# Kernel tuning notes

Measured on AMD Instinct MI355X. Metric: run time of the kernel, lower is better.

## Reference

```python
import jax, jax.numpy as jnp
import numpy as np
from jax import lax

B, T, C, H, W = 2, 32, 8, 192, 192


def _conv(x, w, b):
    y = lax.conv_general_dilated(x, w, (1, 1), 'SAME',
                                 dimension_numbers=('NCHW', 'OIHW', 'NCHW'))
    return y + b[None, :, None, None]


def _interaction(x, c1w, c1b, c2w, c2b, c3w, c3b):
    x = jax.nn.silu(_conv(x, c1w, c1b))
    x = jax.nn.silu(_conv(x, c2w, c2b))
    return _conv(x, c3w, c3b)


def _constrain(xf, ky, kx, k2):
    # xf: [B,T,C,H,Wf] complex; divergence-free projection on channels 0 (u) and 1 (v)
    u = xf[:, :, 0]
    v = xf[:, :, 1]
    div = (ky[:, None] * u + kx[None, :] * v) / k2
    xf = xf.at[:, :, 0].set(u - ky[:, None] * div)
    xf = xf.at[:, :, 1].set(v - kx[None, :] * div)
    return xf


def setup_inputs() -> dict:
    key = jax.random.key(0)
    ks = jax.random.split(key, 8)
    f32 = jnp.float32
    return {
        'x_seq': jax.random.normal(ks[0], (B, T, C, H, W), f32),
        'dt': jax.random.uniform(ks[1], (B,), f32) * 0.1 + 0.01,
        'w1': jax.random.normal(ks[2], (2, 64), f32) * 0.02,
        'b1': jnp.zeros((64,), f32),
        'w2': jax.random.normal(ks[3], (64, C), f32) * 0.02,
        'b2': jnp.zeros((C,), f32),
        'c1w': jax.random.normal(ks[4], (2 * C, C, 3, 3), f32) * 0.05,
        'c1b': jnp.zeros((2 * C,), f32),
        'c2w': jax.random.normal(ks[5], (2 * C, 2 * C, 3, 3), f32) * 0.05,
        'c2b': jnp.zeros((2 * C,), f32),
        'c3w': jax.random.normal(ks[6], (C, 2 * C, 1, 1), f32) * 0.05,
        'c3b': jnp.zeros((C,), f32),
    }


def reference(x_seq, dt, w1, b1, w2, b2, c1w, c1b, c2w, c2b, c3w, c3b):
    Bb, Tt, Cc, Hh, Ww = x_seq.shape
    Wf = Ww // 2 + 1
    ky = jnp.fft.fftfreq(Hh).astype(jnp.float32)
    kx = jnp.fft.rfftfreq(Ww).astype(jnp.float32)
    k2 = ky[:, None] ** 2 + kx[None, :] ** 2
    k2 = k2.at[0, 0].set(1.0)

    # --- learned propagator: A = exp(i * (MLP(k) + |k|) * dt) ---
    kg = jnp.stack(jnp.meshgrid(ky, kx, indexing='ij'), axis=-1).reshape(-1, 2)
    hid = jax.nn.silu(kg @ w1 + b1)
    learned_phase = (hid @ w2 + b2).reshape(Hh, Wf, Cc)
    k_phys = jnp.sqrt(ky[:, None] ** 2 + kx[None, :] ** 2)[..., None]  # [H,Wf,1]
    omega = learned_phase + k_phys
    phase = omega[None] * dt[:, None, None, None]  # [B,H,Wf,C]
    A = lax.complex(jnp.cos(phase), jnp.sin(phase))

    # --- analytical force: grad of interaction-net output sum wrt input ---
    x_flat = x_seq.reshape(Bb * Tt, Cc, Hh, Ww)
    force = jax.grad(lambda xx: _interaction(xx, c1w, c1b, c2w, c2b, c3w, c3b).sum())(x_flat)
    force = force.reshape(Bb, Tt, Cc, Hh, Ww)

    Xf = jnp.fft.rfft2(x_seq + force * dt[:, None, None, None, None],
                       axes=(-2, -1), norm='ortho')  # [B,T,C,H,Wf] complex
    Xf = _constrain(Xf, ky, kx, k2)

    # --- linear recurrence h_t = A*h_{t-1} + X_t via associative scan over T ---
    A_b = jnp.broadcast_to(jnp.transpose(A, (0, 3, 1, 2))[:, None], Xf.shape)

    def comb(e1, e2):
        a1, x1 = e1
        a2, x2 = e2
        return a1 * a2, a2 * x1 + x2

    _, h_f = lax.associative_scan(comb, (A_b, Xf), axis=1)
    h_f = _constrain(h_f, ky, kx, k2)

    # --- energy renormalization ---
    n_in = jnp.sqrt(jnp.sum(jnp.abs(Xf) ** 2, axis=(2, 3, 4), keepdims=True))
    n_out = jnp.sqrt(jnp.sum(jnp.abs(h_f) ** 2, axis=(2, 3, 4), keepdims=True))
    h_f = h_f * (n_in / (n_out + 1e-6))

    return jnp.fft.irfft2(h_f, s=(Hh, Ww), axes=(-2, -1), norm='ortho')
```

## Files before the change

### kernel.cpp

```cpp
#include <hip/hip_runtime.h>
#include <hip/hip_bf16.h>
#include <math.h>

#define HH 192
#define WW 192
#define WF 97
#define NC 8
#define NC2 16
#define NT 32
#define NB 2
#define NIMG (NB*NT)
#define NPLANE (NIMG*NC)
#define PIX (HH*WW)
#define FPIX (HH*WF)
#define NG 13
#define INV_SQRT_N 0.07216878364870322f
#define SCAN_BLOCKS (NB*NC*FPIX/256)

typedef __attribute__((ext_vector_type(8))) short bf16x8;
typedef __attribute__((ext_vector_type(4))) float f32x4;

__device__ inline unsigned short f2bf(float f){
    union { __hip_bfloat16 h; unsigned short u; } cv;
    cv.h = __float2bfloat16(f);
    return cv.u;
}
__device__ inline float bf2f(unsigned short h){
    return __uint_as_float(((unsigned int)h) << 16);
}
__device__ inline float fsigmoid(float y){
    return __builtin_amdgcn_rcpf(1.f + __expf(-y));
}

__global__ void k_tab(float* tw){
    int i = blockIdx.x*blockDim.x + threadIdx.x;
    if (i < 192){
        double ang = 6.283185307179586476925286766559 * (double)i / 192.0;
        tw[i]       = (float)cos(ang);
        tw[192 + i] = (float)sin(ang);
    }
}

__global__ void k_wprep(const float* __restrict__ c1w, const float* __restrict__ c2w,
                        const float* __restrict__ c3w,
                        unsigned short* __restrict__ WT, float* __restrict__ S3){
    int e = blockIdx.x*256 + threadIdx.x;
    if (e < 9216){
        int j  = e & 7;
        int l  = (e >> 3) & 63;
        int fs = e >> 9;
        int px = l & 15, ks = l >> 4;
        float w = 0.f;
        if (fs < 3){
            int tap = 4*fs + ks;
            if (tap < 9) w = c1w[(px*8 + j)*9 + tap];
        } else if (fs < 8){
            int s = fs - 3, tap = 2*s + (ks>>1);
            int ch = (ks&1)*8 + j;
            if (tap < 9) w = c2w[(px*16 + ch)*9 + tap];
        } else if (fs < 13){
            int s = fs - 8, tb = 2*s + (ks>>1);
            int c2 = (ks&1)*8 + j;
            if (tb < 9) w = c2w[(c2*16 + px)*9 + (8 - tb)];
        } else {
            int s = fs - 13, tb = 2*s + (ks>>1);
            int cin = (ks&1)*8 + j;
            if (tb < 9 && px < 8) w = c1w[(cin*8 + px)*9 + (8 - tb)];
        }
        WT[e] = f2bf(w);
    } else if (e < 9232){
        int och = e - 9216;
        float s3 = 0.f;
        for (int q = 0; q < NC; q++) s3 += c3w[q*NC2 + och];
        S3[och] = s3;
    }
}

__global__ void k_A(const float* __restrict__ dt, const float* __restrict__ w1,
                    const float* __restrict__ b1, const float* __restrict__ w2,
                    const float* __restrict__ b2, float* __restrict__ Abuf){
    int idx = blockIdx.x*blockDim.x + threadIdx.x;
    if (idx >= FPIX) return;
    int kyi = idx % HH, kxi = idx / HH;
    float ky = (float)(kyi < 96 ? kyi : kyi - 192) / 192.0f;
    float kx = (float)kxi / 192.0f;
    float lp[NC];
    #pragma unroll
    for (int c = 0; c < NC; c++) lp[c] = b2[c];
    for (int jh = 0; jh < 64; jh++){
        float z  = ky*w1[jh] + kx*w1[64+jh] + b1[jh];
        float sg = 1.0f/(1.0f + expf(-z));
        float h  = z*sg;
        #pragma unroll
        for (int c = 0; c < NC; c++) lp[c] += h * w2[jh*NC + c];
    }
    float kph = sqrtf(ky*ky + kx*kx);
    for (int b = 0; b < NB; b++){
        float d = dt[b];
        #pragma unroll
        for (int c = 0; c < NC; c++){
            float ph = (lp[c] + kph) * d;
            float s, cn;
            sincosf(ph, &s, &cn);
            long o = (((long)(b*NC + c))*FPIX + idx) * 2;
            Abuf[o]   = cn;
            Abuf[o+1] = s;
        }
    }
}

__global__ void k_force(const float* __restrict__ x,
                        const unsigned short* __restrict__ WTu,
                        const float* __restrict__ c1b, const float* __restrict__ c2b,
                        const float* __restrict__ S3,  const float* __restrict__ dt,
                        float* __restrict__ xp){
    __shared__ unsigned short ys1_s[22*22*16];
    __shared__ unsigned short xg2_s[20*20*16];
    int bid = blockIdx.x;
    int tx0 = (bid % 12)*16, ty0 = ((bid/12) % 12)*16;
    int img = bid / 144;
    int tid = threadIdx.x;
    int l = tid & 63, px = l & 15, ks = l >> 4, wv = tid >> 6;
    const bf16x8* wt = (const bf16x8*)WTu;

    unsigned short* xs = xg2_s;
    const float* xb = x + (long)img*NC*PIX;
    for (int pix = tid; pix < 576; pix += 256){
        int sy = pix / 24, sx = pix % 24;
        int gy = ty0 - 4 + sy, gx = tx0 - 4 + sx;
        bool vld = (gy >= 0 && gy < HH && gx >= 0 && gx < WW);
        long gp = (long)gy*WW + gx;
        ushort4 o0, o1;
        #pragma unroll
        for (int c = 0; c < 8; c++){
            float v = vld ? xb[c*PIX + gp] : 0.f;
            unsigned short h = f2bf(v);
            if (c < 4) ((unsigned short*)&o0)[c] = h;
            else       ((unsigned short*)&o1)[c-4] = h;
        }
        *(ushort4*)(xs + pix*8)     = o0;
        *(ushort4*)(xs + pix*8 + 4) = o1;
    }
    __syncthreads();

    ushort4 dy1r[6];
    {
        bf16x8 a0 = wt[0*64 + l], a1 = wt[1*64 + l], a2 = wt[2*64 + l];
        float b1v[4];
        #pragma unroll
        for (int r = 0; r < 4; r++) b1v[r] = c1b[ks*4 + r];
        int t0 = (0 + ks < 9) ? ks : 8;
        int t1 = (4 + ks < 9) ? 4 + ks : 8;
        int t2 = 8;
        int o0 = ((t0/3)*24 + t0%3)*8, o1 = ((t1/3)*24 + t1%3)*8, o2 = ((t2/3)*24 + t2%3)*8;
        #pragma unroll
        for (int i = 0; i < 6; i++){
            int g = wv + 4*i;
            if (g < 21){
                int p = g*16 + px;
                int pc = (p < 324) ? p : 323;
                int ry = pc/18, rx = pc%18;
                const unsigned short* bp = xs + ((ry+2)*24 + rx+2)*8;
                f32x4 acc = {0.f,0.f,0.f,0.f};
                acc = __builtin_amdgcn_mfma_f32_16x16x32_bf16(a0, *(const bf16x8*)(bp+o0), acc, 0,0,0);
                acc = __builtin_amdgcn_mfma_f32_16x16x32_bf16(a1, *(const bf16x8*)(bp+o1), acc, 0,0,0);
                acc = __builtin_amdgcn_mfma_f32_16x16x32_bf16(a2, *(const bf16x8*)(bp+o2), acc, 0,0,0);
                int gy = ty0 - 1 + ry, gx = tx0 - 1 + rx;
                bool vld = (gy >= 0 && gy < HH && gx >= 0 && gx < WW);
                ushort4 yo, dyo;
                #pragma unroll
                for (int r = 0; r < 4; r++){
                    float yv = acc[r] + b1v[r];
                    float sg = fsigmoid(yv);
                    ((unsigned short*)&yo)[r]  = vld ? f2bf(yv*sg) : (unsigned short)0;
                    ((unsigned short*)&dyo)[r] = vld ? f2bf(sg*(1.f + yv*(1.f - sg)))
                                                     : (unsigned short)0;
                }
                dy1r[i] = dyo;
                if (p < 324)
                    *(ushort4*)(ys1_s + ((ry+2)*22 + rx+2)*16 + ks*4) = yo;
            }
        }
        #pragma unroll
        for (int i = 0; i < 3; i++){
            int g = wv + 4*i;
            if (g < 10){
                int p = g*16 + px;
                int oy, ox;
                if (p < 88){ int q = p/22; oy = (q < 2) ? q : q + 18; ox = p - q*22; }
                else { int rr = p - 88; oy = (rr>>2) + 2; int c4 = rr & 3;
                       ox = (c4 < 2) ? c4 : c4 + 18; }
                const unsigned short* bp = xs + (oy*24 + ox)*8;
                f32x4 acc = {0.f,0.f,0.f,0.f};
                acc = __builtin_amdgcn_mfma_f32_16x16x32_bf16(a0, *(const bf16x8*)(bp+o0), acc, 0,0,0);
                acc = __builtin_amdgcn_mfma_f32_16x16x32_bf16(a1, *(const bf16x8*)(bp+o1), acc, 0,0,0);
                acc = __builtin_amdgcn_mfma_f32_16x16x32_bf16(a2, *(const bf16x8*)(bp+o2), acc, 0,0,0);
                int gy = ty0 - 3 + oy, gx = tx0 - 3 + ox;
                bool vld = (gy >= 0 && gy < HH && gx >= 0 && gx < WW);
                ushort4 yo;
                #pragma unroll
                for (int r = 0; r < 4; r++){
                    float yv = acc[r] + b1v[r];
                    float sg = fsigmoid(yv);
                    ((unsigned short*)&yo)[r] = vld ? f2bf(yv*sg) : (unsigned short)0;
                }
                *(ushort4*)(ys1_s + (oy*22 + ox)*16 + ks*4) = yo;
            }
        }
    }
    __syncthreads();

    unsigned short* g2s = xg2_s;
    {
        bf16x8 a0 = wt[3*64+l], a1 = wt[4*64+l], a2 = wt[5*64+l],
               a3 = wt[6*64+l], a4 = wt[7*64+l];
        float b2v[4], s3v[4];
        #pragma unroll
        for (int r = 0; r < 4; r++){ b2v[r] = c2b[ks*4+r]; s3v[r] = S3[ks*4+r]; }
        int hb = (ks&1)*8;
        int toff[5];
        #pragma unroll
        for (int s = 0; s < 5; s++){
            int tap = 2*s + (ks>>1); int t = (tap < 9) ? tap : 8;
            toff[s] = ((t/3)*22 + t%3)*16 + hb;
        }
        #pragma unroll
        for (int i = 0; i < 7; i++){
            int g = wv + 4*i;
            if (g < 25){
                int p = g*16 + px;
                int qy = p/20, qx = p%20;
                const unsigned short* bp = ys1_s + (qy*22 + qx)*16;
                f32x4 acc = {0.f,0.f,0.f,0.f};
                acc = __builtin_amdgcn_mfma_f32_16x16x32_bf16(a0, *(const bf16x8*)(bp+toff[0]), acc, 0,0,0);
                acc = __builtin_amdgcn_mfma_f32_16x16x32_bf16(a1, *(const bf16x8*)(bp+toff[1]), acc, 0,0,0);
                acc = __builtin_amdgcn_mfma_f32_16x16x32_bf16(a2, *(const bf16x8*)(bp+toff[2]), acc, 0,0,0);
                acc = __builtin_amdgcn_mfma_f32_16x16x32_bf16(a3, *(const bf16x8*)(bp+toff[3]), acc, 0,0,0);
                acc = __builtin_amdgcn_mfma_f32_16x16x32_bf16(a4, *(const bf16x8*)(bp+toff[4]), acc, 0,0,0);
                int gy = ty0 - 2 + qy, gx = tx0 - 2 + qx;
                bool vld = (gy >= 0 && gy < HH && gx >= 0 && gx < WW);
                ushort4 go;
                #pragma unroll
                for (int r = 0; r < 4; r++){
                    float yv = acc[r] + b2v[r];
                    float sg = fsigmoid(yv);
                    float ds = sg*(1.f + yv*(1.f - sg));
                    ((unsigned short*)&go)[r] = vld ? f2bf(ds * s3v[r]) : (unsigned short)0;
                }
                *(ushort4*)(g2s + p*16 + ks*4) = go;
            }
        }
    }
    __syncthreads();

    unsigned short* g1s = ys1_s;
    {
        bf16x8 a0 = wt[8*64+l], a1 = wt[9*64+l], a2 = wt[10*64+l],
               a3 = wt[11*64+l], a4 = wt[12*64+l];
        int hb = (ks&1)*8;
        int toff[5];
        #pragma unroll
        for (int s = 0; s < 5; s++){
            int tb = 2*s + (ks>>1); int t = (tb < 9) ? tb : 8;
            toff[s] = ((2-(t/3))*20 + 2-(t%3))*16 + hb;
        }
        #pragma unroll
        for (int i = 0; i < 6; i++){
            int g = wv + 4*i;
            if (g < 21){
                int p = g*16 + px;
                int pc = (p < 324) ? p : 323;
                int ry = pc/18, rx = pc%18;
                const unsigned short* bp = g2s + (ry*20 + rx)*16;
                f32x4 acc = {0.f,0.f,0.f,0.f};
                acc = __builtin_amdgcn_mfma_f32_16x16x32_bf16(a0, *(const bf16x8*)(bp+toff[0]), acc, 0,0,0);
                acc = __builtin_amdgcn_mfma_f32_16x16x32_bf16(a1, *(const bf16x8*)(bp+toff[1]), acc, 0,0,0);
                acc = __builtin_amdgcn_mfma_f32_16x16x32_bf16(a2, *(const bf16x8*)(bp+toff[2]), acc, 0,0,0);
                acc = __builtin_amdgcn_mfma_f32_16x16x32_bf16(a3, *(const bf16x8*)(bp+toff[3]), acc, 0,0,0);
                acc = __builtin_amdgcn_mfma_f32_16x16x32_bf16(a4, *(const bf16x8*)(bp+toff[4]), acc, 0,0,0);
                if (p < 324){
                    ushort4 dv = dy1r[i];
                    ushort4 go;
                    #pragma unroll
                    for (int r = 0; r < 4; r++){
                        float v = acc[r] * bf2f(((unsigned short*)&dv)[r]);
                        ((unsigned short*)&go)[r] = f2bf(v);
                    }
                    *(ushort4*)(g1s + p*16 + ks*4) = go;
                }
            }
        }
    }
    __syncthreads();

    {
        bf16x8 a0 = wt[13*64+l], a1 = wt[14*64+l], a2 = wt[15*64+l],
               a3 = wt[16*64+l], a4 = wt[17*64+l];
        int hb = (ks&1)*8;
        int toff[5];
        #pragma unroll
        for (int s = 0; s < 5; s++){
            int tb = 2*s + (ks>>1); int t = (tb < 9) ? tb : 8;
            toff[s] = ((2-(t/3))*18 + 2-(t%3))*16 + hb;
        }
        float d = dt[img / NT];
        #pragma unroll
        for (int i = 0; i < 4; i++){
            int y = wv + 4*i;
            const unsigned short* bp = g1s + (y*18 + px)*16;
            f32x4 acc = {0.f,0.f,0.f,0.f};
            acc = __builtin_amdgcn_mfma_f32_16x16x32_bf16(a0, *(const bf16x8*)(bp+toff[0]), acc, 0,0,0);
            acc = __builtin_amdgcn_mfma_f32_16x16x32_bf16(a1, *(const bf16x8*)(bp+toff[1]), acc, 0,0,0);
            acc = __builtin_amdgcn_mfma_f32_16x16x32_bf16(a2, *(const bf16x8*)(bp+toff[2]), acc, 0,0,0);
            acc = __builtin_amdgcn_mfma_f32_16x16x32_bf16(a3, *(const bf16x8*)(bp+toff[3]), acc, 0,0,0);
            acc = __builtin_amdgcn_mfma_f32_16x16x32_bf16(a4, *(const bf16x8*)(bp+toff[4]), acc, 0,0,0);
            if (ks < 2){
                int gpix = (ty0+y)*WW + (tx0+px);
                #pragma unroll
                for (int r = 0; r < 4; r++){
                    int c = ks*4 + r;
                    long gi = ((long)img*NC + c)*PIX + gpix;
                    xp[gi] = x[gi] + d*acc[r];
                }
            }
        }
    }
}

__global__ void k_rowfft2(const float* __restrict__ xp, const float* __restrict__ tw,
                          float* __restrict__ R){
    __shared__ float2 bufC[1728];
    __shared__ float2 bufA[1836];
    __shared__ float twc[192], tws[192];
    int p  = blockIdx.x / 12;
    int r0 = (blockIdx.x % 12)*16;
    int t  = threadIdx.x;
    twc[t] = tw[t]; tws[t] = tw[192+t];
    const float* base = xp + (long)p*PIX + (long)r0*WW;
    #pragma unroll
    for (int jj = 0; jj < 8; jj++){
        float2 z; z.x = base[(2*jj)*WW + t]; z.y = base[(2*jj+1)*WW + t];
        bufC[t*9 + jj] = z;
    }
    __syncthreads();
    int k1 = t / 12, n2 = t % 12;
    {
        float wr[16], wi[16];
        int m = (n2*k1) % 192, step = (12*k1) % 192;
        #pragma unroll
        for (int n1 = 0; n1 < 16; n1++){
            wr[n1] = twc[m]; wi[n1] = -tws[m];
            m += step; if (m >= 192) m -= 192;
        }
        #pragma unroll
        for (int jj = 0; jj < 8; jj++){
            float re = 0.f, im = 0.f;
            #pragma unroll
            for (int n1 = 0; n1 < 16; n1++){
                float2 v = bufC[(12*n1 + n2)*9 + jj];
                re += v.x*wr[n1] - v.y*wi[n1];
                im += v.x*wi[n1] + v.y*wr[n1];
            }
            float2 a; a.x = re; a.y = im;
            bufA[(n2*17 + k1)*9 + jj] = a;
        }
    }
    __syncthreads();
    {
        int kk1 = t % 16, k2 = t / 16;
        float wr[12], wi[12];
        int m = 0, step = (16*k2) % 192;
        #pragma unroll
        for (int q = 0; q < 12; q++){
            wr[q] = twc[m]; wi[q] = -tws[m];
            m += step; if (m >= 192) m -= 192;
        }
        #pragma unroll
        for (int jj = 0; jj < 8; jj++){
            float re = 0.f, im = 0.f;
            #pragma unroll
            for (int q = 0; q < 12; q++){
                float2 a = bufA[(q*17 + kk1)*9 + jj];
                re += a.x*wr[q] - a.y*wi[q];
                im += a.x*wi[q] + a.y*wr[q];
            }
            float2 z; z.x = re*INV_SQRT_N; z.y = im*INV_SQRT_N;
            bufC[t*9 + jj] = z;
        }
    }
    __syncthreads();
    if (t < WF){
        int t2 = (t == 0) ? 0 : 192 - t;
        #pragma unroll
        for (int jj = 0; jj < 8; jj++){
            float2 u = bufC[t*9 + jj], v = bufC[t2*9 + jj];
            float2 A_; A_.x = 0.5f*(u.x + v.x); A_.y = 0.5f*(u.y - v.y);
            float2 B_; B_.x = 0.5f*(u.y + v.y); B_.y = -0.5f*(u.x - v.x);
            bufA[t*17 + 2*jj]     = A_;
            bufA[t*17 + 2*jj + 1] = B_;
        }
    }
    __syncthreads();
    float2* dst = ((float2*)R) + (long)p*FPIX + r0;
    for (int idx = t; idx < 97*16; idx += 192){
        int kx = idx >> 4, ry = idx & 15;
        dst[(long)kx*HH + ry] = bufA[kx*17 + ry];
    }
}

__global__ void k_invrow2(const float* __restrict__ G, const float* __restrict__ tw,
                          float* __restrict__ out){
    __shared__ float2 bufC[1728];
    __shared__ float2 bufA[1836];
    __shared__ float twc[192], tws[192];
    int p  = blockIdx.x / 12;
    int r0 = (blockIdx.x % 12)*16;
    int t  = threadIdx.x;
    twc[t] = tw[t]; tws[t] = tw[192+t];
    const float2* Gb = ((const float2*)G) + (long)p*FPIX + r0;
    for (int idx = t; idx < 97*16; idx += 192){
        int kx = idx >> 4, ry = idx & 15;
        bufA[kx*17 + ry] = Gb[(long)kx*HH + ry];
    }
    __syncthreads();
    int tt = (t <= 96) ? t : 192 - t;
    bool dcny = (t == 0) || (t == 96);
    #pragma unroll
    for (int jj = 0; jj < 8; jj++){
        float2 a = bufA[tt*17 + 2*jj];
        float2 b = bufA[tt*17 + 2*jj + 1];
        if (dcny){ a.y = 0.f; b.y = 0.f; }
        float2 z;
        if (t <= 96){ z.x = a.x - b.y; z.y = a.y + b.x; }
        else        { z.x = a.x + b.y; z.y = b.x - a.y; }
        bufC[t*9 + jj] = z;
    }
    __syncthreads();
    int k1 = t / 12, n2 = t % 12;
    {
        float wr[16], wi[16];
        int m = (n2*k1) % 192, step = (12*k1) % 192;
        #pragma unroll
        for (int n1 = 0; n1 < 16; n1++){
            wr[n1] = twc[m]; wi[n1] = tws[m];
            m += step; if (m >= 192) m -= 192;
        }
        #pragma unroll
        for (int jj = 0; jj < 8; jj++){
            float re = 0.f, im = 0.f;
            #pragma unroll
            for (int n1 = 0; n1 < 16; n1++){
                float2 v = bufC[(12*n1 + n2)*9 + jj];
                re += v.x*wr[n1] - v.y*wi[n1];
                im += v.x*wi[n1] + v.y*wr[n1];
            }
            float2 a; a.x = re; a.y = im;
            bufA[(n2*17 + k1)*9 + jj] = a;
        }
    }
    __syncthreads();
    {
        int kk1 = t % 16, k2 = t / 16;
        float wr[12], wi[12];
        int m = 0, step = (16*k2) % 192;
        #pragma unroll
        for (int q = 0; q < 12; q++){
            wr[q] = twc[m]; wi[q] = tws[m];
            m += step; if (m >= 192) m -= 192;
        }
        float* ob = out + (long)p*PIX + (long)r0*WW;
        #pragma unroll
        for (int jj = 0; jj < 8; jj++){
            float re = 0.f, im = 0.f;
            #pragma unroll
            for (int q = 0; q < 12; q++){
                float2 a = bufA[(q*17 + kk1)*9 + jj];
                re += a.x*wr[q] - a.y*wi[q];
                im += a.x*wi[q] + a.y*wr[q];
            }
            ob[(2*jj)*WW + t]   = re*INV_SQRT_N;
            ob[(2*jj+1)*WW + t] = im*INV_SQRT_N;
        }
    }
}

template<int DIRSGN, bool RESCALE>
__global__ void k_cfft(const float* __restrict__ in, const float* __restrict__ tw,
                       const float* __restrict__ nrm, float* __restrict__ out){
    __shared__ float2 C[HH][9];
    __shared__ float2 A1[12][17][9];
    __shared__ float twc[192], tws[192];
    const float sgn = (DIRSGN > 0) ? 1.f : -1.f;
    int p  = blockIdx.x / NG;
    int g  = blockIdx.x % NG;
    int j0 = g*8;
    int t  = threadIdx.x;
    twc[t] = tw[t]; tws[t] = tw[192+t];
    float scale = 1.f;
    if (RESCALE){
        int bt = p / NC;
        scale = sqrtf(nrm[bt]) / (sqrtf(nrm[64+bt]) + 1e-6f);
    }
    const float2* src = ((const float2*)in) + (long)p*FPIX;
    #pragma unroll
    for (int jj = 0; jj < 8; jj++){
        float2 v = {0.f, 0.f};
        if (j0 + jj < WF) v = src[(long)(j0+jj)*HH + t];
        v.x *= scale; v.y *= scale;
        C[t][jj] = v;
    }
    __syncthreads();
    {
        int k1 = t / 12, n2 = t % 12;
        float wr[16], wi[16];
        int m = (n2*k1) % 192, step = (12*k1) % 192;
        #pragma unroll
        for (int n1 = 0; n1 < 16; n1++){
            wr[n1] = twc[m]; wi[n1] = sgn*tws[m];
            m += step; if (m >= 192) m -= 192;
        }
        #pragma unroll
        for (int jj = 0; jj < 8; jj++){
            float re = 0.f, im = 0.f;
            #pragma unroll
            for (int n1 = 0; n1 < 16; n1++){
                float2 v = C[12*n1 + n2][jj];
                re += v.x*wr[n1] - v.y*wi[n1];
                im += v.x*wi[n1] + v.y*wr[n1];
            }
            float2 a; a.x = re; a.y = im;
            A1[n2][k1][jj] = a;
        }
    }
    __syncthreads();
    {
        int k1 = t % 16, k2 = t / 16;
        float wr[12], wi[12];
        int m = 0, step = (16*k2) % 192;
        #pragma unroll
        for (int n2 = 0; n2 < 12; n2++){
            wr[n2] = twc[m]; wi[n2] = sgn*tws[m];
            m += step; if (m >= 192) m -= 192;
        }
        float2* dst = ((float2*)out) + (long)p*FPIX;
        #pragma unroll
        for (int jj = 0; jj < 8; jj++){
            float re = 0.f, im = 0.f;
            #pragma unroll
            for (int n2 = 0; n2 < 12; n2++){
                float2 a = A1[n2][k1][jj];
                re += a.x*wr[n2] - a.y*wi[n2];
                im += a.x*wi[n2] + a.y*wr[n2];
            }
            if (j0 + jj < WF){
                float2 r; r.x = re*INV_SQRT_N; r.y = im*INV_SQRT_N;
                dst[(long)(j0+jj)*HH + t] = r;
            }
        }
    }
}

__global__ void k_scan(const float* __restrict__ Xf, const float* __restrict__ Abuf,
                       float* __restrict__ Hf, float* __restrict__ scr){
    __shared__ float part[64];
    int tid = threadIdx.x;
    if (tid < 64) part[tid] = 0.f;
    __syncthreads();
    int idx = blockIdx.x*256 + tid;
    int f = idx % FPIX; int tmp = idx / FPIX;
    int c = tmp % NC; int b = tmp / NC;
    int lane0 = ((tid & 63) == 0);
    if (c == 0){
        int kyi = f % HH, kxi = f / HH;
        float ky = (float)(kyi < 96 ? kyi : kyi - 192)/192.0f;
        float kx = (float)kxi/192.0f;
        float k2 = ky*ky + kx*kx;
        if (f == 0) k2 = 1.0f;
        float rk2 = 1.0f/k2;
        long a0 = (((long)(b*NC + 0))*FPIX + f)*2;
        long a1 = (((long)(b*NC + 1))*FPIX + f)*2;
        float A0r = Abuf[a0], A0i = Abuf[a0+1];
        float A1r = Abuf[a1], A1i = Abuf[a1+1];
        float h0r = 0.f, h0i = 0.f, h1r = 0.f, h1i = 0.f;
        for (int t = 0; t < NT; t++){
            long e0 = (((((long)b*NT + t)*NC + 0)*FPIX) + f)*2;
            long e1 = (((((long)b*NT + t)*NC + 1)*FPIX) + f)*2;
            float ur = Xf[e0], ui = Xf[e0+1];
            float vr = Xf[e1], vi = Xf[e1+1];
            float pr = (ky*ur + kx*vr)*rk2;
            float pi = (ky*ui + kx*vi)*rk2;
            ur -= ky*pr; ui -= ky*pi;
            vr -= kx*pr; vi -= kx*pi;
            float nin = ur*ur + ui*ui + vr*vr + vi*vi;
            float n0r = A0r*h0r - A0i*h0i + ur;
            float n0i = A0r*h0i + A0i*h0r + ui;
            float n1r = A1r*h1r - A1i*h1i + vr;
            float n1i = A1r*h1i + A1i*h1r + vi;
            h0r = n0r; h0i = n0i; h1r = n1r; h1i = n1i;
            float dr = (ky*h0r + kx*h1r)*rk2;
            float di = (ky*h0i + kx*h1i)*rk2;
            float o0r = h0r - ky*dr, o0i = h0i - ky*di;
            float o1r = h1r - kx*dr, o1i = h1i - kx*di;
            Hf[e0] = o0r; Hf[e0+1] = o0i;
            Hf[e1] = o1r; Hf[e1+1] = o1i;
            float nout = o0r*o0r + o0i*o0i + o1r*o1r + o1i*o1i;
            #pragma unroll
            for (int off = 32; off > 0; off >>= 1){
                nin  += __shfl_xor(nin,  off);
                nout += __shfl_xor(nout, off);
            }
            if (lane0){
                atomicAdd(&part[t],      nin);
                atomicAdd(&part[32 + t], nout);
            }
        }
    } else if (c != 1){
        long ao = (((long)(b*NC + c))*FPIX + f)*2;
        float ar = Abuf[ao], ai = Abuf[ao+1];
        float hr = 0.0f, hi = 0.0f;
        for (int t = 0; t < NT; t++){
            long e = (((((long)b*NT + t)*NC + c)*FPIX) + f)*2;
            float xr = Xf[e], xi = Xf[e+1];
            float nin = xr*xr + xi*xi;
            float nr = ar*hr - ai*hi + xr;
            float ni = ar*hi + ai*hr + xi;
            hr = nr; hi = ni;
            Hf[e] = hr; Hf[e+1] = hi;
            float nout = hr*hr + hi*hi;
            #pragma unroll
            for (int off = 32; off > 0; off >>= 1){
                nin  += __shfl_xor(nin,  off);
                nout += __shfl_xor(nout, off);
            }
            if (lane0){
                atomicAdd(&part[t],      nin);
                atomicAdd(&part[32 + t], nout);
            }
        }
    }
    __syncthreads();
    if (tid < 64) scr[(long)blockIdx.x*64 + tid] = part[tid];
}

__global__ void k_nred(const float* __restrict__ scr, float* __restrict__ nrm){
    int o = threadIdx.x;
    int io = o >> 6;
    int bt = o & 63;
    int b = bt >> 5, t = bt & 31;
    const int BPB = SCAN_BLOCKS/NB;
    float s = 0.f;
    for (int blk = 0; blk < BPB; blk++)
        s += scr[((long)(b*BPB + blk))*64 + io*32 + t];
    nrm[io*64 + bt] = s;
}

extern "C" void kernel_launch(void* const* d_in, const int* in_sizes, int n_in,
                              void* d_out, int out_size, void* d_ws, size_t ws_size,
                              hipStream_t stream){
    const float* x   = (const float*)d_in[0];
    const float* dt  = (const float*)d_in[1];
    const float* w1  = (const float*)d_in[2];
    const float* b1  = (const float*)d_in[3];
    const float* w2  = (const float*)d_in[4];
    const float* b2  = (const float*)d_in[5];
    const float* c1w = (const float*)d_in[6];
    const float* c1b = (const float*)d_in[7];
    const float* c2w = (const float*)d_in[8];
    const float* c2b = (const float*)d_in[9];
    const float* c3w = (const float*)d_in[10];
    float* out = (float*)d_out;
    float* ws  = (float*)d_ws;

    const long RSZ = (long)NPLANE*FPIX*2;
    float* R1  = ws;
    float* R2  = ws + RSZ;
    float* AB  = R2 + RSZ;
    float* TW  = AB + (long)NB*NC*FPIX*2;
    float* NRM = TW + 384;
    float* WTf = NRM + 128;
    unsigned short* WT = (unsigned short*)WTf;
    float* S3  = WTf + 4608;
    float* SCR = S3 + 16;

    k_tab<<<2, 128, 0, stream>>>(TW);
    k_wprep<<<37, 256, 0, stream>>>(c1w, c2w, c3w, WT, S3);
    k_A<<<(FPIX + 255)/256, 256, 0, stream>>>(dt, w1, b1, w2, b2, AB);

    k_force<<<NIMG*144, 256, 0, stream>>>(x, WT, c1b, c2b, S3, dt, out);

    k_rowfft2<<<NPLANE*12, 192, 0, stream>>>(out, TW, R1);
    k_cfft<-1,false><<<NPLANE*NG, 192, 0, stream>>>(R1, TW, NRM, R2);
    k_scan<<<SCAN_BLOCKS, 256, 0, stream>>>(R2, AB, R1, SCR);
    k_nred<<<1, 128, 0, stream>>>(SCR, NRM);
    k_cfft<+1,true><<<NPLANE*NG, 192, 0, stream>>>(R1, TW, NRM, R2);
    k_invrow2<<<NPLANE*12, 192, 0, stream>>>(R2, TW, out);
}
```

Measured before the change: 604.9 us.

## Precompute per-thread twiddle tables and process two frequencies per scan thread

Adds a kernel that precomputes, for each forward/inverse direction, the per-thread twiddle factors used by the row and column FFT kernels. The FFT kernels now load them as coalesced float2 reads from global memory instead of staging cos/sin tables in shared memory and walking modular indices. The scan kernel now handles two adjacent frequencies per thread with float4 loads and stores, halving the thread count and widening memory accesses. This costs extra global twiddle traffic and more registers per scan thread, which lowers the number of scan blocks.

```diff
diff --git a/kernel.cpp b/kernel.cpp
--- a/kernel.cpp
+++ b/kernel.cpp
@@ -13,9 +13,10 @@
 #define NPLANE (NIMG*NC)
 #define PIX (HH*WW)
 #define FPIX (HH*WF)
+#define HP (FPIX/2)
 #define NG 13
 #define INV_SQRT_N 0.07216878364870322f
-#define SCAN_BLOCKS (NB*NC*FPIX/256)
+#define SCAN_BLOCKS (NB*NC*HP/256)
 
 typedef __attribute__((ext_vector_type(8))) short bf16x8;
 typedef __attribute__((ext_vector_type(4))) float f32x4;
@@ -39,6 +40,18 @@
         tw[i]       = (float)cos(ang);
         tw[192 + i] = (float)sin(ang);
     }
+}
+
+__global__ void k_twt(const float* __restrict__ tw, float2* __restrict__ twt){
+    int e = blockIdx.x*256 + threadIdx.x;
+    if (e >= 10752) return;
+    int t = e % 192; int s = (e/192) % 28; int d = e / (192*28);
+    float sgn = d ? 1.f : -1.f;
+    int m;
+    if (s < 16){ int k1 = t/12, n2 = t%12; m = (n2*k1 + 12*k1*s) % 192; }
+    else       { int q = s - 16; int k2 = t/16; m = (16*k2*q) % 192; }
+    float2 w; w.x = tw[m]; w.y = sgn*tw[192 + m];
+    twt[(d*28 + s)*192 + t] = w;
 }
 
 __global__ void k_wprep(const float* __restrict__ c1w, const float* __restrict__ c2w,
@@ -327,15 +340,13 @@
     }
 }
 
-__global__ void k_rowfft2(const float* __restrict__ xp, const float* __restrict__ tw,
+__global__ void k_rowfft2(const float* __restrict__ xp, const float2* __restrict__ twt,
                           float* __restrict__ R){
     __shared__ float2 bufC[1728];
     __shared__ float2 bufA[1836];
-    __shared__ float twc[192], tws[192];
     int p  = blockIdx.x / 12;
     int r0 = (blockIdx.x % 12)*16;
     int t  = threadIdx.x;
-    twc[t] = tw[t]; tws[t] = tw[192+t];
     const float* base = xp + (long)p*PIX + (long)r0*WW;
     #pragma unroll
     for (int jj = 0; jj < 8; jj++){
@@ -346,11 +357,10 @@
     int k1 = t / 12, n2 = t % 12;
     {
         float wr[16], wi[16];
-        int m = (n2*k1) % 192, step = (12*k1) % 192;
         #pragma unroll
         for (int n1 = 0; n1 < 16; n1++){
-            wr[n1] = twc[m]; wi[n1] = -tws[m];
-            m += step; if (m >= 192) m -= 192;
+            float2 w = twt[n1*192 + t];
+            wr[n1] = w.x; wi[n1] = w.y;
         }
         #pragma unroll
         for (int jj = 0; jj < 8; jj++){
@@ -367,13 +377,12 @@
     }
     __syncthreads();
     {
-        int kk1 = t % 16, k2 = t / 16;
+        int kk1 = t % 16;
         float wr[12], wi[12];
-        int m = 0, step = (16*k2) % 192;
         #pragma unroll
         for (int q = 0; q < 12; q++){
-            wr[q] = twc[m]; wi[q] = -tws[m];
-            m += step; if (m >= 192) m -= 192;
+            float2 w = twt[(16+q)*192 + t];
+            wr[q] = w.x; wi[q] = w.y;
         }
         #pragma unroll
         for (int jj = 0; jj < 8; jj++){
@@ -408,15 +417,13 @@
     }
 }
 
-__global__ void k_invrow2(const float* __restrict__ G, const float* __restrict__ tw,
+__global__ void k_invrow2(const float* __restrict__ G, const float2* __restrict__ twt,
                           float* __restrict__ out){
     __shared__ float2 bufC[1728];
     __shared__ float2 bufA[1836];
-    __shared__ float twc[192], tws[192];
     int p  = blockIdx.x / 12;
     int r0 = (blockIdx.x % 12)*16;
     int t  = threadIdx.x;
-    twc[t] = tw[t]; tws[t] = tw[192+t];
     const float2* Gb = ((const float2*)G) + (long)p*FPIX + r0;
     for (int idx = t; idx < 97*16; idx += 192){
         int kx = idx >> 4, ry = idx & 15;
@@ -437,13 +444,13 @@
     }
     __syncthreads();
     int k1 = t / 12, n2 = t % 12;
+    const float2* T = twt + 28*192;
     {
         float wr[16], wi[16];
-        int m = (n2*k1) % 192, step = (12*k1) % 192;
         #pragma unroll
         for (int n1 = 0; n1 < 16; n1++){
-            wr[n1] = twc[m]; wi[n1] = tws[m];
-            m += step; if (m >= 192) m -= 192;
+            float2 w = T[n1*192 + t];
+            wr[n1] = w.x; wi[n1] = w.y;
         }
         #pragma unroll
         for (int jj = 0; jj < 8; jj++){
@@ -460,13 +467,12 @@
     }
     __syncthreads();
     {
-        int kk1 = t % 16, k2 = t / 16;
+        int kk1 = t % 16;
         float wr[12], wi[12];
-        int m = 0, step = (16*k2) % 192;
         #pragma unroll
         for (int q = 0; q < 12; q++){
-            wr[q] = twc[m]; wi[q] = tws[m];
-            m += step; if (m >= 192) m -= 192;
+            float2 w = T[(16+q)*192 + t];
+            wr[q] = w.x; wi[q] = w.y;
         }
         float* ob = out + (long)p*PIX + (long)r0*WW;
         #pragma unroll
@@ -485,17 +491,15 @@
 }
 
 template<int DIRSGN, bool RESCALE>
-__global__ void k_cfft(const float* __restrict__ in, const float* __restrict__ tw,
+__global__ void k_cfft(const float* __restrict__ in, const float2* __restrict__ twt,
                        const float* __restrict__ nrm, float* __restrict__ out){
     __shared__ float2 C[HH][9];
     __shared__ float2 A1[12][17][9];
-    __shared__ float twc[192], tws[192];
-    const float sgn = (DIRSGN > 0) ? 1.f : -1.f;
+    const int DIRI = (DIRSGN > 0) ? 1 : 0;
     int p  = blockIdx.x / NG;
     int g  = blockIdx.x % NG;
     int j0 = g*8;
     int t  = threadIdx.x;
-    twc[t] = tw[t]; tws[t] = tw[192+t];
     float scale = 1.f;
     if (RESCALE){
         int bt = p / NC;
@@ -510,14 +514,14 @@
         C[t][jj] = v;
     }
     __syncthreads();
+    const float2* T = twt + DIRI*28*192;
     {
         int k1 = t / 12, n2 = t % 12;
         float wr[16], wi[16];
-        int m = (n2*k1) % 192, step = (12*k1) % 192;
         #pragma unroll
         for (int n1 = 0; n1 < 16; n1++){
-            wr[n1] = twc[m]; wi[n1] = sgn*tws[m];
-            m += step; if (m >= 192) m -= 192;
+            float2 w = T[n1*192 + t];
+            wr[n1] = w.x; wi[n1] = w.y;
         }
         #pragma unroll
         for (int jj = 0; jj < 8; jj++){
@@ -534,23 +538,22 @@
     }
     __syncthreads();
     {
-        int k1 = t % 16, k2 = t / 16;
+        int k1 = t % 16;
         float wr[12], wi[12];
-        int m = 0, step = (16*k2) % 192;
-        #pragma unroll
-        for (int n2 = 0; n2 < 12; n2++){
-            wr[n2] = twc[m]; wi[n2] = sgn*tws[m];
-            m += step; if (m >= 192) m -= 192;
+        #pragma unroll
+        for (int q = 0; q < 12; q++){
+            float2 w = T[(16+q)*192 + t];
+            wr[q] = w.x; wi[q] = w.y;
         }
         float2* dst = ((float2*)out) + (long)p*FPIX;
         #pragma unroll
         for (int jj = 0; jj < 8; jj++){
             float re = 0.f, im = 0.f;
             #pragma unroll
-            for (int n2 = 0; n2 < 12; n2++){
-                float2 a = A1[n2][k1][jj];
-                re += a.x*wr[n2] - a.y*wi[n2];
-                im += a.x*wi[n2] + a.y*wr[n2];
+            for (int q = 0; q < 12; q++){
+                float2 a = A1[q][k1][jj];
+                re += a.x*wr[q] - a.y*wi[q];
+                im += a.x*wi[q] + a.y*wr[q];
             }
             if (j0 + jj < WF){
                 float2 r; r.x = re*INV_SQRT_N; r.y = im*INV_SQRT_N;
@@ -567,43 +570,64 @@
     if (tid < 64) part[tid] = 0.f;
     __syncthreads();
     int idx = blockIdx.x*256 + tid;
-    int f = idx % FPIX; int tmp = idx / FPIX;
+    int u = idx % HP; int tmp = idx / HP;
     int c = tmp % NC; int b = tmp / NC;
+    int f0 = 2*u;
     int lane0 = ((tid & 63) == 0);
     if (c == 0){
-        int kyi = f % HH, kxi = f / HH;
-        float ky = (float)(kyi < 96 ? kyi : kyi - 192)/192.0f;
-        float kx = (float)kxi/192.0f;
-        float k2 = ky*ky + kx*kx;
-        if (f == 0) k2 = 1.0f;
-        float rk2 = 1.0f/k2;
-        long a0 = (((long)(b*NC + 0))*FPIX + f)*2;
-        long a1 = (((long)(b*NC + 1))*FPIX + f)*2;
-        float A0r = Abuf[a0], A0i = Abuf[a0+1];
-        float A1r = Abuf[a1], A1i = Abuf[a1+1];
-        float h0r = 0.f, h0i = 0.f, h1r = 0.f, h1i = 0.f;
+        int ky0i = f0 % HH, kxi = f0 / HH;
+        float ky0 = (float)(ky0i < 96 ? ky0i : ky0i - 192)/192.0f;
+        int ky1i = ky0i + 1;
+        float ky1 = (float)(ky1i < 96 ? ky1i : ky1i - 192)/192.0f;
+        float kx_ = (float)kxi/192.0f;
+        float k20 = ky0*ky0 + kx_*kx_; if (f0 == 0) k20 = 1.0f;
+        float k21 = ky1*ky1 + kx_*kx_;
+        float rk20 = 1.0f/k20, rk21 = 1.0f/k21;
+        long a0 = (((long)(b*NC + 0))*FPIX + f0)*2;
+        long a1 = (((long)(b*NC + 1))*FPIX + f0)*2;
+        float4 A0 = *(const float4*)(Abuf + a0);
+        float4 A1v = *(const float4*)(Abuf + a1);
+        float h0r0=0.f,h0i0=0.f,h1r0=0.f,h1i0=0.f;
+        float h0r1=0.f,h0i1=0.f,h1r1=0.f,h1i1=0.f;
         for (int t = 0; t < NT; t++){
-            long e0 = (((((long)b*NT + t)*NC + 0)*FPIX) + f)*2;
-            long e1 = (((((long)b*NT + t)*NC + 1)*FPIX) + f)*2;
-            float ur = Xf[e0], ui = Xf[e0+1];
-            float vr = Xf[e1], vi = Xf[e1+1];
-            float pr = (ky*ur + kx*vr)*rk2;
-            float pi = (ky*ui + kx*vi)*rk2;
-            ur -= ky*pr; ui -= ky*pi;
-            vr -= kx*pr; vi -= kx*pi;
+            long e0 = (((((long)b*NT + t)*NC + 0)*FPIX) + f0)*2;
+            long e1 = (((((long)b*NT + t)*NC + 1)*FPIX) + f0)*2;
+            float4 U = *(const float4*)(Xf + e0);
+            float4 V = *(const float4*)(Xf + e1);
+            float ur = U.x, ui = U.y, vr = V.x, vi = V.y;
+            float pr = (ky0*ur + kx_*vr)*rk20;
+            float pi = (ky0*ui + kx_*vi)*rk20;
+            ur -= ky0*pr; ui -= ky0*pi; vr -= kx_*pr; vi -= kx_*pi;
             float nin = ur*ur + ui*ui + vr*vr + vi*vi;
-            float n0r = A0r*h0r - A0i*h0i + ur;
-            float n0i = A0r*h0i + A0i*h0r + ui;
-            float n1r = A1r*h1r - A1i*h1i + vr;
-            float n1i = A1r*h1i + A1i*h1r + vi;
-            h0r = n0r; h0i = n0i; h1r = n1r; h1i = n1i;
-            float dr = (ky*h0r + kx*h1r)*rk2;
-            float di = (ky*h0i + kx*h1i)*rk2;
-            float o0r = h0r - ky*dr, o0i = h0i - ky*di;
-            float o1r = h1r - kx*dr, o1i = h1i - kx*di;
-            Hf[e0] = o0r; Hf[e0+1] = o0i;
-            Hf[e1] = o1r; Hf[e1+1] = o1i;
+            float n0r = A0.x*h0r0 - A0.y*h0i0 + ur;
+            float n0i = A0.x*h0i0 + A0.y*h0r0 + ui;
+            float n1r = A1v.x*h1r0 - A1v.y*h1i0 + vr;
+            float n1i = A1v.x*h1i0 + A1v.y*h1r0 + vi;
+            h0r0 = n0r; h0i0 = n0i; h1r0 = n1r; h1i0 = n1i;
+            float dr = (ky0*h0r0 + kx_*h1r0)*rk20;
+            float di = (ky0*h0i0 + kx_*h1i0)*rk20;
+            float o0r = h0r0 - ky0*dr, o0i = h0i0 - ky0*di;
+            float o1r = h1r0 - kx_*dr, o1i = h1i0 - kx_*di;
             float nout = o0r*o0r + o0i*o0i + o1r*o1r + o1i*o1i;
+            float ur1 = U.z, ui1 = U.w, vr1 = V.z, vi1 = V.w;
+            float pr1 = (ky1*ur1 + kx_*vr1)*rk21;
+            float pi1 = (ky1*ui1 + kx_*vi1)*rk21;
+            ur1 -= ky1*pr1; ui1 -= ky1*pi1; vr1 -= kx_*pr1; vi1 -= kx_*pi1;
+            nin += ur1*ur1 + ui1*ui1 + vr1*vr1 + vi1*vi1;
+            float m0r = A0.z*h0r1 - A0.w*h0i1 + ur1;
+            float m0i = A0.z*h0i1 + A0.w*h0r1 + ui1;
+            float m1r = A1v.z*h1r1 - A1v.w*h1i1 + vr1;
+            float m1i = A1v.z*h1i1 + A1v.w*h1r1 + vi1;
+            h0r1 = m0r; h0i1 = m0i; h1r1 = m1r; h1i1 = m1i;
+            float dr1 = (ky1*h0r1 + kx_*h1r1)*rk21;
+            float di1 = (ky1*h0i1 + kx_*h1i1)*rk21;
+            float q0r = h0r1 - ky1*dr1, q0i = h0i1 - ky1*di1;
+            float q1r = h1r1 - kx_*dr1, q1i = h1i1 - kx_*di1;
+            nout += q0r*q0r + q0i*q0i + q1r*q1r + q1i*q1i;
+            float4 O0; O0.x = o0r; O0.y = o0i; O0.z = q0r; O0.w = q0i;
+            float4 O1; O1.x = o1r; O1.y = o1i; O1.z = q1r; O1.w = q1i;
+            *(float4*)(Hf + e0) = O0;
+            *(float4*)(Hf + e1) = O1;
             #pragma unroll
             for (int off = 32; off > 0; off >>= 1){
                 nin  += __shfl_xor(nin,  off);
@@ -615,18 +639,21 @@
             }
         }
     } else if (c != 1){
-        long ao = (((long)(b*NC + c))*FPIX + f)*2;
-        float ar = Abuf[ao], ai = Abuf[ao+1];
-        float hr = 0.0f, hi = 0.0f;
+        long ao = (((long)(b*NC + c))*FPIX + f0)*2;
+        float4 A = *(const float4*)(Abuf + ao);
+        float hr0 = 0.f, hi0 = 0.f, hr1 = 0.f, hi1 = 0.f;
         for (int t = 0; t < NT; t++){
-            long e = (((((long)b*NT + t)*NC + c)*FPIX) + f)*2;
-            float xr = Xf[e], xi = Xf[e+1];
-            float nin = xr*xr + xi*xi;
-            float nr = ar*hr - ai*hi + xr;
-            float ni = ar*hi + ai*hr + xi;
-            hr = nr; hi = ni;
-            Hf[e] = hr; Hf[e+1] = hi;
-            float nout = hr*hr + hi*hi;
+            long e = (((((long)b*NT + t)*NC + c)*FPIX) + f0)*2;
+            float4 X = *(const float4*)(Xf + e);
+            float nin = X.x*X.x + X.y*X.y + X.z*X.z + X.w*X.w;
+            float nr0 = A.x*hr0 - A.y*hi0 + X.x;
+            float ni0 = A.x*hi0 + A.y*hr0 + X.y;
+            float nr1 = A.z*hr1 - A.w*hi1 + X.z;
+            float ni1 = A.z*hi1 + A.w*hr1 + X.w;
+            hr0 = nr0; hi0 = ni0; hr1 = nr1; hi1 = ni1;
+            float4 O; O.x = hr0; O.y = hi0; O.z = hr1; O.w = hi1;
+            *(float4*)(Hf + e) = O;
+            float nout = hr0*hr0 + hi0*hi0 + hr1*hr1 + hi1*hi1;
             #pragma unroll
             for (int off = 32; off > 0; off >>= 1){
                 nin  += __shfl_xor(nin,  off);
@@ -681,17 +708,19 @@
     unsigned short* WT = (unsigned short*)WTf;
     float* S3  = WTf + 4608;
     float* SCR = S3 + 16;
+    float2* TWT = (float2*)(SCR + SCAN_BLOCKS*64);
 
     k_tab<<<2, 128, 0, stream>>>(TW);
+    k_twt<<<42, 256, 0, stream>>>(TW, TWT);
     k_wprep<<<37, 256, 0, stream>>>(c1w, c2w, c3w, WT, S3);
     k_A<<<(FPIX + 255)/256, 256, 0, stream>>>(dt, w1, b1, w2, b2, AB);
 
     k_force<<<NIMG*144, 256, 0, stream>>>(x, WT, c1b, c2b, S3, dt, out);
 
-    k_rowfft2<<<NPLANE*12, 192, 0, stream>>>(out, TW, R1);
-    k_cfft<-1,false><<<NPLANE*NG, 192, 0, stream>>>(R1, TW, NRM, R2);
+    k_rowfft2<<<NPLANE*12, 192, 0, stream>>>(out, TWT, R1);
+    k_cfft<-1,false><<<NPLANE*NG, 192, 0, stream>>>(R1, TWT, NRM, R2);
     k_scan<<<SCAN_BLOCKS, 256, 0, stream>>>(R2, AB, R1, SCR);
     k_nred<<<1, 128, 0, stream>>>(SCR, NRM);
-    k_cfft<+1,true><<<NPLANE*NG, 192, 0, stream>>>(R1, TW, NRM, R2);
-    k_invrow2<<<NPLANE*12, 192, 0, stream>>>(R2, TW, out);
-}
+    k_cfft<+1,true><<<NPLANE*NG, 192, 0, stream>>>(R1, TWT, NRM, R2);
+    k_invrow2<<<NPLANE*12, 192, 0, stream>>>(R2, TWT, out);
+}
```

New measurement: 596.7 us. No clear change (-1.4%).
